# Performance work log

Hardware: AMD Instinct MI355X
Metric: run time of the kernel (lower is better)

## Reference

```python
import jax, jax.numpy as jnp
import numpy as np

K = 20
SLOPE = 0.2  # LeakyReLU negative slope used by DGCNN edge convs


def _knn_idx(x, k):
    # x: [C, N]. Returns [N, k] indices of nearest neighbors by L2 distance
    # (includes self), matching torch topk of -pairwise_dist.
    xx = jnp.sum(x * x, axis=0)                      # [N]
    neg_dist = 2.0 * (x.T @ x) - xx[:, None] - xx[None, :]  # [N, N]
    return jax.lax.top_k(neg_dist, k)[1]


def _graph_feature(x, k):
    # x: [C, N] -> edge features [2C, N, k] = concat(x_j - x_i, x_i)
    idx = _knn_idx(x, k)                             # [N, k]
    nb = x[:, idx]                                   # [C, N, k] gather
    xc = jnp.broadcast_to(x[:, :, None], nb.shape)   # [C, N, k]
    return jnp.concatenate([nb - xc, xc], axis=0)


def _edge_conv(x, w, s, c, k):
    # 1x1 Conv2d (no bias) + eval-mode BN folded into per-channel (s, c)
    # + LeakyReLU, then max over the k neighbors.
    f = _graph_feature(x, k)                         # [2C, N, k]
    y = jnp.einsum('oc,cnk->onk', w, f)              # [Co, N, k]
    y = jax.nn.leaky_relu(y * s[:, None, None] + c[:, None, None], SLOPE)
    return jnp.max(y, axis=-1)                       # [Co, N]


def setup_inputs() -> dict:
    key = jax.random.key(0)
    ks = jax.random.split(key, 25)
    N = 16384
    f32 = jnp.float32

    def w(k, shape):
        return jax.random.normal(k, shape, dtype=f32) * 0.05

    def scale(k, shape):
        return 1.0 + 0.1 * jax.random.uniform(k, shape, dtype=f32)

    return {
        'coords': jax.random.normal(ks[0], (N, 3), dtype=f32),
        'feats': jax.random.uniform(ks[1], (N, 1), dtype=f32),
        'w1': w(ks[2], (64, 8)),    's1': scale(ks[3], (64,)),  'c1': w(ks[4], (64,)),
        'w2': w(ks[5], (64, 128)),  's2': scale(ks[6], (64,)),  'c2': w(ks[7], (64,)),
        'w3': w(ks[8], (128, 128)), 's3': scale(ks[9], (128,)), 'c3': w(ks[10], (128,)),
        'w4': w(ks[11], (256, 256)),'s4': scale(ks[12], (256,)),'c4': w(ks[13], (256,)),
        'w5': w(ks[14], (512, 512)),'s5': scale(ks[15], (512,)),'c5': w(ks[16], (512,)),
        'wf': w(ks[17], (3, 256, 512)), 'sf': scale(ks[18], (3, 256)), 'cf': w(ks[19], (3, 256)),
        'wsem': w(ks[20], (20, 256)), 'bsem': w(ks[21], (20,)),
    }


def reference(coords, feats, w1, s1, c1, w2, s2, c2, w3, s3, c3,
              w4, s4, c4, w5, s5, c5, wf, sf, cf, wsem, bsem):
    # Single-cloud batch (batch_size=1): x_input = cat(coords, feats).T -> [4, N]
    x0 = jnp.concatenate([coords.T, feats.T], axis=0)        # [4, N]
    x1 = _edge_conv(x0, w1, s1, c1, K)                       # [64, N]
    x2 = _edge_conv(x1, w2, s2, c2, K)                       # [64, N]
    x3 = _edge_conv(x2, w3, s3, c3, K)                       # [128, N]
    x4 = _edge_conv(x3, w4, s4, c4, K)                       # [256, N]
    cat = jnp.concatenate([x1, x2, x3, x4], axis=0)          # [512, N]
    x5 = jax.nn.leaky_relu(
        jnp.einsum('oc,cn->on', w5, cat) * s5[:, None] + c5[:, None], SLOPE)

    # Multi-scale feat_layers + out_bn (eval-mode BN folded to sf, cf)
    ms_feats = (jnp.einsum('soc,cn->son', wf, x5)
                * sf[:, :, None] + cf[:, :, None])           # [3, 256, N]

    # sem_head on the last scale's features
    sem_feat = ms_feats[-1].T                                # [N, 256]
    sem_logits = (sem_feat @ wsem.T + bsem)[None]            # [1, N, 20]

    ms_coords = jnp.broadcast_to(coords[None], (3,) + coords.shape)  # [3, N, 3]
    ms_masks = jnp.zeros((3, coords.shape[0]), dtype=bool)           # [3, N]
    return ms_feats, ms_coords, ms_masks, sem_logits
```

## Files before the change

kernel.cpp:

```cpp
#include <hip/hip_runtime.h>
#include <hip/hip_bf16.h>
#include <cmath>

#define K_NN 20
#define SLOPE 0.2f
#define NSEG 8
#define TK 16
#define SCAP 8

__device__ __forceinline__ float lrelu(float x) { return x > 0.f ? x : SLOPE * x; }

__device__ __forceinline__ void topk_insert(float (&bd)[K_NN], int (&bi)[K_NN], float nd, int ji) {
  bool c[K_NN];
#pragma unroll
  for (int j = 0; j < K_NN; ++j) c[j] = nd > bd[j];
#pragma unroll
  for (int j = K_NN - 1; j >= 1; --j) {
    bd[j] = c[j] ? (c[j - 1] ? bd[j - 1] : nd) : bd[j];
    bi[j] = c[j] ? (c[j - 1] ? bi[j - 1] : ji) : bi[j];
  }
  bd[0] = c[0] ? nd : bd[0];
  bi[0] = c[0] ? ji : bi[0];
}

__global__ void build_x0_coords(const float* __restrict__ coords, const float* __restrict__ feats,
                                float* __restrict__ x0, float* __restrict__ oC,
                                float* __restrict__ oM, int N) {
  int n = blockIdx.x * 256 + threadIdx.x;
  if (n >= N) return;
  float c0 = coords[n * 3 + 0], c1 = coords[n * 3 + 1], c2 = coords[n * 3 + 2];
  float f = feats[n];
  float4 v = make_float4(c0, c1, c2, f);
  *(float4*)(x0 + (size_t)n * 4) = v;
#pragma unroll
  for (int s = 0; s < 3; ++s) {
    size_t b = (size_t)s * N * 3 + (size_t)n * 3;
    oC[b + 0] = c0; oC[b + 1] = c1; oC[b + 2] = c2;
    oM[(size_t)s * N + n] = 0.f;
  }
}

__global__ void compute_xx(const float* __restrict__ x, int ld, int C,
                           float* __restrict__ xx, int N) {
  int n = blockIdx.x * 256 + threadIdx.x;
  if (n >= N) return;
  const float* r = x + (size_t)n * ld;
  float s = 0.f;
  for (int c = 0; c < C; c += 4) {
    float4 v = *(const float4*)(r + c);
    s += v.x * v.x; s += v.y * v.y; s += v.z * v.z; s += v.w * v.w;
  }
  xx[n] = s;
}

template <int C>
__global__ __launch_bounds__(256, 2) void knn_seg(
    const float* __restrict__ xP, int ld, const float* __restrict__ xx,
    float* __restrict__ pd, int* __restrict__ pi, int N, int segLen) {
  constexpr int T = 64;
  __shared__ float tile[T * C];
  __shared__ float txx[T];
  __shared__ float sd_st[SCAP * 256];
  __shared__ int si_st[SCAP * 256];
  int tid = threadIdx.x;
  int q = blockIdx.x * 256 + tid;
  int j0 = blockIdx.y * segLen;

  float4 qv[C / 4];
#pragma unroll
  for (int c4 = 0; c4 < C / 4; ++c4) qv[c4] = *(const float4*)(xP + (size_t)q * ld + c4 * 4);
  float xxq = xx[q];

  float bd[K_NN]; int bi[K_NN];
#pragma unroll
  for (int k = 0; k < K_NN; ++k) { bd[k] = -INFINITY; bi[k] = 0; }
  float thr = -INFINITY;
  int cnt = 0;

  for (int jt = j0; jt < j0 + segLen; jt += T) {
    constexpr int TOT4 = T * C / 4;
    for (int f = tid; f < TOT4; f += 256) {
      int t = f / (C / 4), c4 = f % (C / 4);
      *(float4*)(tile + t * C + c4 * 4) = *(const float4*)(xP + (size_t)(jt + t) * ld + c4 * 4);
    }
    if (tid < T) txx[tid] = xx[jt + tid];
    __syncthreads();
#pragma unroll 2
    for (int t = 0; t < T; ++t) {
      const float4* rp = (const float4*)(tile + t * C);
      float dot = 0.f;
#pragma unroll
      for (int c4 = 0; c4 < C / 4; ++c4) {
        float4 v = rp[c4];
        dot += qv[c4].x * v.x; dot += qv[c4].y * v.y;
        dot += qv[c4].z * v.z; dot += qv[c4].w * v.w;
      }
      float nd = 2.f * dot - xxq - txx[t];
      if (nd > thr) {
        sd_st[cnt * 256 + tid] = nd;
        si_st[cnt * 256 + tid] = jt + t;
        cnt++;
      }
      if (__any(cnt == SCAP)) {
        for (int e = 0; e < cnt; ++e) {
          float dnd = sd_st[e * 256 + tid];
          int dji = si_st[e * 256 + tid];
          if (dnd > bd[K_NN - 1]) topk_insert(bd, bi, dnd, dji);
        }
        cnt = 0;
        thr = bd[K_NN - 1];
      }
    }
    __syncthreads();
  }
  for (int e = 0; e < cnt; ++e) {
    float dnd = sd_st[e * 256 + tid];
    int dji = si_st[e * 256 + tid];
    if (dnd > bd[K_NN - 1]) topk_insert(bd, bi, dnd, dji);
  }

  size_t base = ((size_t)blockIdx.y * N + q) * K_NN;
#pragma unroll
  for (int k = 0; k < K_NN; ++k) { pd[base + k] = bd[k]; pi[base + k] = bi[k]; }
}

__global__ void knn_merge(const float* __restrict__ pd, const int* __restrict__ pi,
                          int* __restrict__ idx, int N, int S) {
  int q = blockIdx.x * 256 + threadIdx.x;
  if (q >= N) return;
  float bd[K_NN]; int bi[K_NN];
#pragma unroll
  for (int k = 0; k < K_NN; ++k) { bd[k] = -INFINITY; bi[k] = 0; }
  for (int s = 0; s < S; ++s) {
    size_t base = ((size_t)s * N + q) * K_NN;
    for (int k = 0; k < K_NN; ++k) {
      float nd = pd[base + k];
      if (!(nd > bd[K_NN - 1])) break;
      topk_insert(bd, bi, nd, pi[base + k]);
    }
  }
#pragma unroll
  for (int k = 0; k < K_NN; ++k) idx[(size_t)q * K_NN + k] = bi[k];
}

__global__ void prep_wcat(const float* __restrict__ w, float* __restrict__ wcat, int O, int C) {
  int i = blockIdx.x * 256 + threadIdx.x;
  if (i >= O * C) return;
  int o = i / C, c = i % C;
  float wa = w[(size_t)o * 2 * C + c];
  float wb = w[(size_t)o * 2 * C + C + c];
  wcat[(size_t)o * C + c] = wa;
  wcat[((size_t)O + o) * C + c] = wb - wa;
}

template <int MODE>
__global__ __launch_bounds__(256) void gemm_nt(
    const float* __restrict__ A, int lda, const float* __restrict__ B, int ldb,
    float* __restrict__ Out, int ldo, int M, int Nout, int Kdim,
    const float* __restrict__ sv, const float* __restrict__ cv) {
  __shared__ float As[TK][64];
  __shared__ float Bs[TK][64];
  int tid = threadIdx.x;
  int tx = tid & 15, ty = tid >> 4;
  int m0 = blockIdx.x * 64, n0 = blockIdx.y * 64;
  int lrow = tid >> 2, lkq = tid & 3;
  float acc[4][4] = {};

  for (int k0 = 0; k0 < Kdim; k0 += TK) {
    float4 av = make_float4(0.f, 0.f, 0.f, 0.f), bv = make_float4(0.f, 0.f, 0.f, 0.f);
    if (k0 + lkq * 4 < Kdim) {
      av = *(const float4*)(A + (size_t)(m0 + lrow) * lda + k0 + lkq * 4);
      bv = *(const float4*)(B + (size_t)(n0 + lrow) * ldb + k0 + lkq * 4);
    }
    As[lkq * 4 + 0][lrow] = av.x; As[lkq * 4 + 1][lrow] = av.y;
    As[lkq * 4 + 2][lrow] = av.z; As[lkq * 4 + 3][lrow] = av.w;
    Bs[lkq * 4 + 0][lrow] = bv.x; Bs[lkq * 4 + 1][lrow] = bv.y;
    Bs[lkq * 4 + 2][lrow] = bv.z; Bs[lkq * 4 + 3][lrow] = bv.w;
    __syncthreads();
#pragma unroll
    for (int kk = 0; kk < TK; ++kk) {
      float a[4], b[4];
      *(float4*)a = *(const float4*)&As[kk][ty * 4];
      *(float4*)b = *(const float4*)&Bs[kk][tx * 4];
#pragma unroll
      for (int i = 0; i < 4; ++i)
#pragma unroll
        for (int j = 0; j < 4; ++j) acc[i][j] += a[i] * b[j];
    }
    __syncthreads();
  }

  float4 s4 = make_float4(1.f, 1.f, 1.f, 1.f), c4 = make_float4(0.f, 0.f, 0.f, 0.f);
  if (MODE != 0) {
    s4 = *(const float4*)(sv + n0 + tx * 4);
    c4 = *(const float4*)(cv + n0 + tx * 4);
  }
#pragma unroll
  for (int i = 0; i < 4; ++i) {
    float4 r = make_float4(acc[i][0], acc[i][1], acc[i][2], acc[i][3]);
    if (MODE != 0) {
      r.x = r.x * s4.x + c4.x; r.y = r.y * s4.y + c4.y;
      r.z = r.z * s4.z + c4.z; r.w = r.w * s4.w + c4.w;
    }
    if (MODE == 1) { r.x = lrelu(r.x); r.y = lrelu(r.y); r.z = lrelu(r.z); r.w = lrelu(r.w); }
    *(float4*)(Out + (size_t)(m0 + ty * 4 + i) * ldo + n0 + tx * 4) = r;
  }
}

template <int O>
__global__ void edge_max(const float* __restrict__ U, const int* __restrict__ idx,
                         const float* __restrict__ sv, const float* __restrict__ cv,
                         float* __restrict__ out, int N) {
  constexpr int TPP = O / 4;
  constexpr int PPB = 256 / TPP;
  int tid = threadIdx.x;
  int n = blockIdx.x * PPB + tid / TPP;
  int o4 = tid % TPP;
  const int* ir = idx + (size_t)n * K_NN;
  float4 m = make_float4(-INFINITY, -INFINITY, -INFINITY, -INFINITY);
#pragma unroll
  for (int k = 0; k < K_NN; ++k) {
    int j = ir[k];
    float4 t = *(const float4*)(U + (size_t)j * (2 * O) + o4 * 4);
    m.x = fmaxf(m.x, t.x); m.y = fmaxf(m.y, t.y);
    m.z = fmaxf(m.z, t.z); m.w = fmaxf(m.w, t.w);
  }
  float4 v = *(const float4*)(U + (size_t)n * (2 * O) + O + o4 * 4);
  float4 s4 = *(const float4*)(sv + o4 * 4);
  float4 c4 = *(const float4*)(cv + o4 * 4);
  float4 r;
  r.x = lrelu(s4.x * (v.x + m.x) + c4.x);
  r.y = lrelu(s4.y * (v.y + m.y) + c4.y);
  r.z = lrelu(s4.z * (v.z + m.z) + c4.z);
  r.w = lrelu(s4.w * (v.w + m.w) + c4.w);
  *(float4*)(out + (size_t)n * 512 + o4 * 4) = r;
}

__global__ void transpose_nt(const float* __restrict__ in, float* __restrict__ out, int N, int Cc) {
  __shared__ float t[32][33];
  int bx = blockIdx.x, by = blockIdx.y;
  int lx = threadIdx.x, ly = threadIdx.y;
#pragma unroll
  for (int i = 0; i < 4; ++i)
    t[ly + i * 8][lx] = in[(size_t)(by * 32 + ly + i * 8) * Cc + bx * 32 + lx];
  __syncthreads();
#pragma unroll
  for (int i = 0; i < 4; ++i)
    out[(size_t)(bx * 32 + ly + i * 8) * N + by * 32 + lx] = t[lx][ly + i * 8];
}

__global__ void sem_kernel(const float* __restrict__ T1, const float* __restrict__ wsem,
                           const float* __restrict__ bsem, float* __restrict__ out, int N) {
  int tid = threadIdx.x;
  int n = blockIdx.x * 8 + (tid >> 5);
  int g = tid & 31;
  if (g < 20) {
    const float* row = T1 + (size_t)n * 768 + 512;
    const float* wr = wsem + (size_t)g * 256;
    float acc = 0.f;
    for (int o = 0; o < 256; ++o) acc += row[o] * wr[o];
    out[(size_t)n * 20 + g] = acc + bsem[g];
  }
}

template <int C, int O>
static void run_layer(const float* x, int ld, const float* wc, const float* sv, const float* cv,
                      float* outcol, float* xxb, int* idxb, float* pd, int* pi, float* U,
                      int N, hipStream_t stream) {
  compute_xx<<<N / 256, 256, 0, stream>>>(x, ld, C, xxb, N);
  knn_seg<C><<<dim3(N / 256, NSEG), 256, 0, stream>>>(x, ld, xxb, pd, pi, N, N / NSEG);
  knn_merge<<<N / 256, 256, 0, stream>>>(pd, pi, idxb, N, NSEG);
  gemm_nt<0><<<dim3(N / 64, (2 * O) / 64), 256, 0, stream>>>(x, ld, wc, C, U, 2 * O, N, 2 * O, C,
                                                             nullptr, nullptr);
  edge_max<O><<<N / (256 / (O / 4)), 256, 0, stream>>>(U, idxb, sv, cv, outcol, N);
}

extern "C" void kernel_launch(void* const* d_in, const int* in_sizes, int n_in,
                              void* d_out, int out_size, void* d_ws, size_t ws_size,
                              hipStream_t stream) {
  const int N = in_sizes[0] / 3;
  const float* coords = (const float*)d_in[0];
  const float* feats  = (const float*)d_in[1];
  const float* w1 = (const float*)d_in[2];
  const float* s1 = (const float*)d_in[3];
  const float* c1 = (const float*)d_in[4];
  const float* w2 = (const float*)d_in[5];
  const float* s2 = (const float*)d_in[6];
  const float* c2 = (const float*)d_in[7];
  const float* w3 = (const float*)d_in[8];
  const float* s3 = (const float*)d_in[9];
  const float* c3 = (const float*)d_in[10];
  const float* w4 = (const float*)d_in[11];
  const float* s4 = (const float*)d_in[12];
  const float* c4 = (const float*)d_in[13];
  const float* w5 = (const float*)d_in[14];
  const float* s5 = (const float*)d_in[15];
  const float* c5 = (const float*)d_in[16];
  const float* wf = (const float*)d_in[17];
  const float* sf = (const float*)d_in[18];
  const float* cf = (const float*)d_in[19];
  const float* wsem = (const float*)d_in[20];
  const float* bsem = (const float*)d_in[21];

  float* base = (float*)d_ws;
  size_t off = 0;
  float* XC  = base + off; off += (size_t)N * 512;
  float* UX5 = base + off; off += (size_t)N * 512;
  float* x0  = base + off; off += (size_t)N * 4;
  float* xxb = base + off; off += (size_t)N;
  int*   idxb = (int*)(base + off); off += (size_t)N * K_NN;
  float* wc1 = base + off; off += 128 * 4;
  float* wc2 = base + off; off += 128 * 64;
  float* wc3 = base + off; off += 256 * 64;
  float* wc4 = base + off; off += 512 * 128;
  float* T1  = base + off; off += (size_t)N * 768;
  float* pd = T1;
  int*   pi = (int*)(T1 + (size_t)NSEG * N * K_NN);

  float* oF = (float*)d_out;
  float* oC = oF + (size_t)3 * 256 * N;
  float* oM = oC + (size_t)3 * N * 3;
  float* oL = oM + (size_t)3 * N;

  build_x0_coords<<<N / 256, 256, 0, stream>>>(coords, feats, x0, oC, oM, N);

  prep_wcat<<<(64 * 4 + 255) / 256, 256, 0, stream>>>(w1, wc1, 64, 4);
  prep_wcat<<<(64 * 64 + 255) / 256, 256, 0, stream>>>(w2, wc2, 64, 64);
  prep_wcat<<<(128 * 64 + 255) / 256, 256, 0, stream>>>(w3, wc3, 128, 64);
  prep_wcat<<<(256 * 128 + 255) / 256, 256, 0, stream>>>(w4, wc4, 256, 128);

  run_layer<4, 64>(x0, 4, wc1, s1, c1, XC + 0, xxb, idxb, pd, pi, UX5, N, stream);
  run_layer<64, 64>(XC + 0, 512, wc2, s2, c2, XC + 64, xxb, idxb, pd, pi, UX5, N, stream);
  run_layer<64, 128>(XC + 64, 512, wc3, s3, c3, XC + 128, xxb, idxb, pd, pi, UX5, N, stream);
  run_layer<128, 256>(XC + 128, 512, wc4, s4, c4, XC + 256, xxb, idxb, pd, pi, UX5, N, stream);

  gemm_nt<1><<<dim3(N / 64, 8), 256, 0, stream>>>(XC, 512, w5, 512, UX5, 512, N, 512, 512, s5, c5);
  gemm_nt<2><<<dim3(N / 64, 12), 256, 0, stream>>>(UX5, 512, wf, 512, T1, 768, N, 768, 512, sf, cf);
  transpose_nt<<<dim3(24, N / 32), dim3(32, 8), 0, stream>>>(T1, oF, N, 768);
  sem_kernel<<<N / 8, 256, 0, stream>>>(T1, wsem, bsem, oL, N);
}
```

Measured before the change: 4.684 ms.

## Add register-tiled shared-memory kNN kernel for high-dimensional edge-conv layers

Adds a knn_tile kernel that computes 64x64 query-candidate distance tiles with a 4x4 register-blocked dot product from swizzled shared memory. Only 64 threads of each block then scan the tile and maintain the running top-k through a staging buffer. Layers 2-4 (C=64/128) use it with 4 segments instead of 8, while layer 1 keeps the old per-query kernel. The aim is to cut global/LDS traffic per distance compared with the one-query-per-thread scan. The risk is that the selection step runs on only a quarter of the threads and becomes serialized.

```diff
diff --git a/kernel.cpp b/kernel.cpp
--- a/kernel.cpp
+++ b/kernel.cpp
@@ -5,6 +5,7 @@
 #define K_NN 20
 #define SLOPE 0.2f
 #define NSEG 8
+#define NSEG_T 4
 #define TK 16
 #define SCAP 8
 
@@ -124,6 +125,106 @@
   for (int k = 0; k < K_NN; ++k) { pd[base + k] = bd[k]; pi[base + k] = bi[k]; }
 }
 
+template <int C>
+__global__ __launch_bounds__(256) void knn_tile(
+    const float* __restrict__ xP, int ld, const float* __restrict__ xx,
+    float* __restrict__ pd, int* __restrict__ pi, int N, int segLen) {
+  constexpr int SQ4 = (C + 4) / 4;
+  __shared__ float4 Qs[64 * SQ4];
+  __shared__ float4 Cs[64 * SQ4];
+  __shared__ float dist[64 * 65];
+  __shared__ float qxx[64];
+  __shared__ float txx[64];
+  __shared__ float sd_st[SCAP * 64];
+  __shared__ int si_st[SCAP * 64];
+
+  int tid = threadIdx.x;
+  int tx = tid & 15, ty = tid >> 4;
+  int q0 = blockIdx.x * 64;
+  int j0 = blockIdx.y * segLen;
+
+  for (int p = tid; p < 64 * (C / 4); p += 256) {
+    int r = p / (C / 4), c4 = p % (C / 4);
+    Qs[r * SQ4 + (c4 ^ ((r >> 2) & 15))] =
+        *(const float4*)(xP + (size_t)(q0 + r) * ld + c4 * 4);
+  }
+  if (tid < 64) qxx[tid] = xx[q0 + tid];
+
+  float bd[K_NN]; int bi[K_NN];
+#pragma unroll
+  for (int k = 0; k < K_NN; ++k) { bd[k] = -INFINITY; bi[k] = 0; }
+  float thr = -INFINITY;
+  int cnt = 0;
+
+  for (int jt = j0; jt < j0 + segLen; jt += 64) {
+    for (int p = tid; p < 64 * (C / 4); p += 256) {
+      int r = p / (C / 4), c4 = p % (C / 4);
+      Cs[r * SQ4 + (c4 ^ ((r >> 2) & 15))] =
+          *(const float4*)(xP + (size_t)(jt + r) * ld + c4 * 4);
+    }
+    if (tid < 64) txx[tid] = xx[jt + tid];
+    __syncthreads();
+
+    float acc[4][4] = {};
+    for (int kc = 0; kc < C / 4; ++kc) {
+      float4 qa[4], ca[4];
+#pragma unroll
+      for (int i = 0; i < 4; ++i) qa[i] = Qs[(ty * 4 + i) * SQ4 + (kc ^ ty)];
+#pragma unroll
+      for (int j = 0; j < 4; ++j) ca[j] = Cs[(tx * 4 + j) * SQ4 + (kc ^ tx)];
+#pragma unroll
+      for (int i = 0; i < 4; ++i)
+#pragma unroll
+        for (int j = 0; j < 4; ++j) {
+          acc[i][j] += qa[i].x * ca[j].x;
+          acc[i][j] += qa[i].y * ca[j].y;
+          acc[i][j] += qa[i].z * ca[j].z;
+          acc[i][j] += qa[i].w * ca[j].w;
+        }
+    }
+#pragma unroll
+    for (int i = 0; i < 4; ++i) {
+      float xq = qxx[ty * 4 + i];
+#pragma unroll
+      for (int j = 0; j < 4; ++j)
+        dist[(ty * 4 + i) * 65 + tx * 4 + j] =
+            2.f * acc[i][j] - xq - txx[tx * 4 + j];
+    }
+    __syncthreads();
+
+    if (tid < 64) {
+      for (int j = 0; j < 64; ++j) {
+        float nd = dist[tid * 65 + j];
+        if (nd > thr) {
+          sd_st[cnt * 64 + tid] = nd;
+          si_st[cnt * 64 + tid] = jt + j;
+          cnt++;
+        }
+        if (__any(cnt == SCAP)) {
+          for (int e = 0; e < cnt; ++e) {
+            float dnd = sd_st[e * 64 + tid];
+            int dji = si_st[e * 64 + tid];
+            if (dnd > bd[K_NN - 1]) topk_insert(bd, bi, dnd, dji);
+          }
+          cnt = 0;
+          thr = bd[K_NN - 1];
+        }
+      }
+    }
+  }
+
+  if (tid < 64) {
+    for (int e = 0; e < cnt; ++e) {
+      float dnd = sd_st[e * 64 + tid];
+      int dji = si_st[e * 64 + tid];
+      if (dnd > bd[K_NN - 1]) topk_insert(bd, bi, dnd, dji);
+    }
+    size_t base = ((size_t)blockIdx.y * N + q0 + tid) * K_NN;
+#pragma unroll
+    for (int k = 0; k < K_NN; ++k) { pd[base + k] = bd[k]; pi[base + k] = bi[k]; }
+  }
+}
+
 __global__ void knn_merge(const float* __restrict__ pd, const int* __restrict__ pi,
                           int* __restrict__ idx, int N, int S) {
   int q = blockIdx.x * 256 + threadIdx.x;
@@ -264,12 +365,24 @@
 }
 
 template <int C, int O>
-static void run_layer(const float* x, int ld, const float* wc, const float* sv, const float* cv,
-                      float* outcol, float* xxb, int* idxb, float* pd, int* pi, float* U,
-                      int N, hipStream_t stream) {
+static void run_layer_seg(const float* x, int ld, const float* wc, const float* sv,
+                          const float* cv, float* outcol, float* xxb, int* idxb, float* pd,
+                          int* pi, float* U, int N, hipStream_t stream) {
   compute_xx<<<N / 256, 256, 0, stream>>>(x, ld, C, xxb, N);
   knn_seg<C><<<dim3(N / 256, NSEG), 256, 0, stream>>>(x, ld, xxb, pd, pi, N, N / NSEG);
   knn_merge<<<N / 256, 256, 0, stream>>>(pd, pi, idxb, N, NSEG);
+  gemm_nt<0><<<dim3(N / 64, (2 * O) / 64), 256, 0, stream>>>(x, ld, wc, C, U, 2 * O, N, 2 * O, C,
+                                                             nullptr, nullptr);
+  edge_max<O><<<N / (256 / (O / 4)), 256, 0, stream>>>(U, idxb, sv, cv, outcol, N);
+}
+
+template <int C, int O>
+static void run_layer_tile(const float* x, int ld, const float* wc, const float* sv,
+                           const float* cv, float* outcol, float* xxb, int* idxb, float* pd,
+                           int* pi, float* U, int N, hipStream_t stream) {
+  compute_xx<<<N / 256, 256, 0, stream>>>(x, ld, C, xxb, N);
+  knn_tile<C><<<dim3(N / 64, NSEG_T), 256, 0, stream>>>(x, ld, xxb, pd, pi, N, N / NSEG_T);
+  knn_merge<<<N / 256, 256, 0, stream>>>(pd, pi, idxb, N, NSEG_T);
   gemm_nt<0><<<dim3(N / 64, (2 * O) / 64), 256, 0, stream>>>(x, ld, wc, C, U, 2 * O, N, 2 * O, C,
                                                              nullptr, nullptr);
   edge_max<O><<<N / (256 / (O / 4)), 256, 0, stream>>>(U, idxb, sv, cv, outcol, N);
@@ -329,10 +442,10 @@
   prep_wcat<<<(128 * 64 + 255) / 256, 256, 0, stream>>>(w3, wc3, 128, 64);
   prep_wcat<<<(256 * 128 + 255) / 256, 256, 0, stream>>>(w4, wc4, 256, 128);
 
-  run_layer<4, 64>(x0, 4, wc1, s1, c1, XC + 0, xxb, idxb, pd, pi, UX5, N, stream);
-  run_layer<64, 64>(XC + 0, 512, wc2, s2, c2, XC + 64, xxb, idxb, pd, pi, UX5, N, stream);
-  run_layer<64, 128>(XC + 64, 512, wc3, s3, c3, XC + 128, xxb, idxb, pd, pi, UX5, N, stream);
-  run_layer<128, 256>(XC + 128, 512, wc4, s4, c4, XC + 256, xxb, idxb, pd, pi, UX5, N, stream);
+  run_layer_seg<4, 64>(x0, 4, wc1, s1, c1, XC + 0, xxb, idxb, pd, pi, UX5, N, stream);
+  run_layer_tile<64, 64>(XC + 0, 512, wc2, s2, c2, XC + 64, xxb, idxb, pd, pi, UX5, N, stream);
+  run_layer_tile<64, 128>(XC + 64, 512, wc3, s3, c3, XC + 128, xxb, idxb, pd, pi, UX5, N, stream);
+  run_layer_tile<128, 256>(XC + 128, 512, wc4, s4, c4, XC + 256, xxb, idxb, pd, pi, UX5, N, stream);
 
   gemm_nt<1><<<dim3(N / 64, 8), 256, 0, stream>>>(XC, 512, w5, 512, UX5, 512, N, 512, 512, s5, c5);
   gemm_nt<2><<<dim3(N / 64, 12), 256, 0, stream>>>(UX5, 512, wf, 512, T1, 768, N, 768, 512, sf, cf);
```

New measurement: 7.235 ms. +54.5%, slower.

## Compute kNN distances with split-fp16 MFMA and fused in-block top-k merge

Applied to the files above, without the earlier changes.

Layers 2-4 now compute kNN dot products on matrix cores, using a three-term fp16 hi/lo split to approximate fp32 accuracy. A new prep kernel builds the hi/lo halves, and the kNN kernel double-buffers swizzled candidate tiles through LDS. Each query's top-k is filtered by a running threshold and merged across the 8 partial lists inside the block, so the separate segment and merge kernels are no longer needed. This targets the scalar fp32 distance compute that dominates kNN time. The cost is extra prep passes and workspace aliasing, plus a small risk of neighbor ordering differing from the fp32 reference on near-ties.

```diff
diff --git a/kernel.cpp b/kernel.cpp
--- a/kernel.cpp
+++ b/kernel.cpp
@@ -7,6 +7,10 @@
 #define NSEG 8
 #define TK 16
 #define SCAP 8
+
+typedef _Float16 h8 __attribute__((ext_vector_type(8)));
+typedef _Float16 h4 __attribute__((ext_vector_type(4)));
+typedef float f4v __attribute__((ext_vector_type(4)));
 
 __device__ __forceinline__ float lrelu(float x) { return x > 0.f ? x : SLOPE * x; }
 
@@ -51,6 +55,23 @@
     s += v.x * v.x; s += v.y * v.y; s += v.z * v.z; s += v.w * v.w;
   }
   xx[n] = s;
+}
+
+template <int C>
+__global__ void prep_hl(const float* __restrict__ x, int ld, _Float16* __restrict__ xh,
+                        _Float16* __restrict__ xl, int N) {
+  constexpr int C4 = C / 4;
+  int i = blockIdx.x * 256 + threadIdx.x;
+  if (i >= N * C4) return;
+  int n = i / C4, c4 = i % C4;
+  float4 v = *(const float4*)(x + (size_t)n * ld + c4 * 4);
+  h4 hh, ll;
+  hh[0] = (_Float16)v.x; ll[0] = (_Float16)(v.x - (float)hh[0]);
+  hh[1] = (_Float16)v.y; ll[1] = (_Float16)(v.y - (float)hh[1]);
+  hh[2] = (_Float16)v.z; ll[2] = (_Float16)(v.z - (float)hh[2]);
+  hh[3] = (_Float16)v.w; ll[3] = (_Float16)(v.w - (float)hh[3]);
+  *(h4*)(xh + (size_t)n * C + c4 * 4) = hh;
+  *(h4*)(xl + (size_t)n * C + c4 * 4) = ll;
 }
 
 template <int C>
@@ -143,6 +164,179 @@
   for (int k = 0; k < K_NN; ++k) idx[(size_t)q * K_NN + k] = bi[k];
 }
 
+template <int C>
+__global__ __launch_bounds__(512, 2) void knn_mfma(
+    const _Float16* __restrict__ xh, const _Float16* __restrict__ xl,
+    const float* __restrict__ xx, int* __restrict__ idx, int N) {
+  constexpr int SLOTS = C / 8;
+  constexpr int SWM = SLOTS - 1;
+  constexpr int NCH = C / 32;
+  constexpr int TILE_UNITS = 2 * 32 * SLOTS;
+  constexpr int UPT = TILE_UNITS / 256;
+  constexpr int STAGE_B = 2 * 2 * TILE_UNITS * 16;
+  constexpr int MERGE_B = 64 * 8 * K_NN * 8;
+  constexpr int LDS_B = (STAGE_B + 32768 > MERGE_B) ? STAGE_B + 32768 : MERGE_B;
+  __shared__ char lds[LDS_B];
+  float* sd_st = (float*)(lds + STAGE_B);
+  int* si_st = (int*)(lds + STAGE_B + 16384);
+
+  int tid = threadIdx.x;
+  int wv = tid >> 6, lane = tid & 63;
+  int qh = wv >> 1, ch = wv & 1;
+  int lj = lane & 15, g = lane >> 4;
+  int q0 = blockIdx.x * 64;
+  int q = q0 + qh * 16 + lj;
+  int chbase = ch * (N / 2);
+  const int NT = (N / 2) / 32;
+
+  h8 bh[NCH], bl[NCH];
+#pragma unroll
+  for (int m = 0; m < NCH; ++m) {
+    bh[m] = *(const h8*)(xh + (size_t)q * C + m * 32 + g * 8);
+    bl[m] = *(const h8*)(xl + (size_t)q * C + m * 32 + g * 8);
+  }
+  float qxx = xx[q];
+
+  float bd[K_NN]; int bi[K_NN];
+#pragma unroll
+  for (int k = 0; k < K_NN; ++k) { bd[k] = -INFINITY; bi[k] = 0; }
+  float thr = -INFINITY;
+  int cnt = 0;
+
+  int cidx = qh * 64 + lane;
+  float4 ldr[UPT];
+
+  auto ldreg = [&](int t) {
+    int jt = chbase + t * 32;
+#pragma unroll
+    for (int u = 0; u < UPT; ++u) {
+      int p = cidx * UPT + u;
+      int part = p / (32 * SLOTS);
+      int row = (p / SLOTS) & 31;
+      int slot = p & SWM;
+      const _Float16* src = part ? xl : xh;
+      ldr[u] = *(const float4*)(src + (size_t)(jt + row) * C + (slot ^ (row & SWM)) * 8);
+    }
+  };
+  auto dswrite = [&](int buf) {
+#pragma unroll
+    for (int u = 0; u < UPT; ++u) {
+      int p = cidx * UPT + u;
+      *(float4*)(lds + ((size_t)(ch * 2 + buf) * TILE_UNITS + p) * 16) = ldr[u];
+    }
+  };
+  auto compute = [&](int buf, int jt) {
+    float cxx[8];
+#pragma unroll
+    for (int s = 0; s < 2; ++s)
+#pragma unroll
+      for (int r = 0; r < 4; ++r) cxx[s * 4 + r] = xx[jt + s * 16 + g * 4 + r];
+    char* tb = lds + (size_t)(ch * 2 + buf) * TILE_UNITS * 16;
+#pragma unroll
+    for (int sub = 0; sub < 2; ++sub) {
+      int row = sub * 16 + lj;
+      h8 ah[NCH], al[NCH];
+#pragma unroll
+      for (int m = 0; m < NCH; ++m) {
+        int su = (m * 4 + g) ^ (row & SWM);
+        ah[m] = *(const h8*)(tb + ((size_t)(0 * 32 + row) * SLOTS + su) * 16);
+        al[m] = *(const h8*)(tb + ((size_t)(1 * 32 + row) * SLOTS + su) * 16);
+      }
+      f4v acc = {0.f, 0.f, 0.f, 0.f};
+#pragma unroll
+      for (int m = 0; m < NCH; ++m)
+        acc = __builtin_amdgcn_mfma_f32_16x16x32_f16(ah[m], bh[m], acc, 0, 0, 0);
+#pragma unroll
+      for (int m = 0; m < NCH; ++m)
+        acc = __builtin_amdgcn_mfma_f32_16x16x32_f16(ah[m], bl[m], acc, 0, 0, 0);
+#pragma unroll
+      for (int m = 0; m < NCH; ++m)
+        acc = __builtin_amdgcn_mfma_f32_16x16x32_f16(al[m], bh[m], acc, 0, 0, 0);
+#pragma unroll
+      for (int r = 0; r < 4; ++r) {
+        float d = 2.f * acc[r] - qxx - cxx[sub * 4 + r];
+        if (d > thr) {
+          sd_st[cnt * 512 + tid] = d;
+          si_st[cnt * 512 + tid] = jt + sub * 16 + g * 4 + r;
+          cnt++;
+        }
+        if (__any(cnt == SCAP)) {
+          for (int e = 0; e < cnt; ++e) {
+            float dnd = sd_st[e * 512 + tid];
+            int dji = si_st[e * 512 + tid];
+            if (dnd > bd[K_NN - 1]) topk_insert(bd, bi, dnd, dji);
+          }
+          cnt = 0;
+          thr = bd[K_NN - 1];
+        }
+      }
+    }
+  };
+
+  ldreg(0);
+  dswrite(0);
+  __syncthreads();
+  for (int t = 0; t < NT; ++t) {
+    int cur = t & 1;
+    if (t + 1 < NT) ldreg(t + 1);
+    compute(cur, chbase + t * 32);
+    __syncthreads();
+    if (t + 1 < NT) {
+      dswrite(cur ^ 1);
+      __syncthreads();
+    }
+  }
+  for (int e = 0; e < cnt; ++e) {
+    float dnd = sd_st[e * 512 + tid];
+    int dji = si_st[e * 512 + tid];
+    if (dnd > bd[K_NN - 1]) topk_insert(bd, bi, dnd, dji);
+  }
+  __syncthreads();
+
+  float* mg = (float*)lds;
+  int list = ch * 4 + g;
+  int qlocal = qh * 16 + lj;
+#pragma unroll
+  for (int k = 0; k < K_NN; ++k) {
+    int e = ((qlocal * 8 + list) * K_NN + k) * 2;
+    mg[e] = bd[k];
+    ((int*)mg)[e + 1] = bi[k];
+  }
+  __syncthreads();
+  if (tid < 64) {
+    int pr[8] = {0, 0, 0, 0, 0, 0, 0, 0};
+    float hd[8]; int hx[8];
+#pragma unroll
+    for (int j = 0; j < 8; ++j) {
+      int e = ((tid * 8 + j) * K_NN) * 2;
+      hd[j] = mg[e]; hx[j] = ((int*)mg)[e + 1];
+    }
+    for (int k = 0; k < K_NN; ++k) {
+      float best = hd[0]; int bidx = hx[0]; int bj = 0;
+#pragma unroll
+      for (int j = 1; j < 8; ++j) {
+        bool btr = (hd[j] > best) || (hd[j] == best && hx[j] < bidx);
+        best = btr ? hd[j] : best;
+        bidx = btr ? hx[j] : bidx;
+        bj = btr ? j : bj;
+      }
+      idx[(size_t)(q0 + tid) * K_NN + k] = bidx;
+#pragma unroll
+      for (int j = 0; j < 8; ++j) {
+        if (j == bj) {
+          pr[j]++;
+          if (pr[j] < K_NN) {
+            int e = ((tid * 8 + j) * K_NN + pr[j]) * 2;
+            hd[j] = mg[e]; hx[j] = ((int*)mg)[e + 1];
+          } else {
+            hd[j] = -INFINITY; hx[j] = 0x7fffffff;
+          }
+        }
+      }
+    }
+  }
+}
+
 __global__ void prep_wcat(const float* __restrict__ w, float* __restrict__ wcat, int O, int C) {
   int i = blockIdx.x * 256 + threadIdx.x;
   if (i >= O * C) return;
@@ -264,12 +458,24 @@
 }
 
 template <int C, int O>
-static void run_layer(const float* x, int ld, const float* wc, const float* sv, const float* cv,
-                      float* outcol, float* xxb, int* idxb, float* pd, int* pi, float* U,
-                      int N, hipStream_t stream) {
+static void run_layer_seg(const float* x, int ld, const float* wc, const float* sv,
+                          const float* cv, float* outcol, float* xxb, int* idxb, float* pd,
+                          int* pi, float* U, int N, hipStream_t stream) {
   compute_xx<<<N / 256, 256, 0, stream>>>(x, ld, C, xxb, N);
   knn_seg<C><<<dim3(N / 256, NSEG), 256, 0, stream>>>(x, ld, xxb, pd, pi, N, N / NSEG);
   knn_merge<<<N / 256, 256, 0, stream>>>(pd, pi, idxb, N, NSEG);
+  gemm_nt<0><<<dim3(N / 64, (2 * O) / 64), 256, 0, stream>>>(x, ld, wc, C, U, 2 * O, N, 2 * O, C,
+                                                             nullptr, nullptr);
+  edge_max<O><<<N / (256 / (O / 4)), 256, 0, stream>>>(U, idxb, sv, cv, outcol, N);
+}
+
+template <int C, int O>
+static void run_layer_mfma(const float* x, int ld, const float* wc, const float* sv,
+                           const float* cv, float* outcol, float* xxb, int* idxb,
+                           _Float16* xh, _Float16* xl, float* U, int N, hipStream_t stream) {
+  compute_xx<<<N / 256, 256, 0, stream>>>(x, ld, C, xxb, N);
+  prep_hl<C><<<(N * (C / 4)) / 256, 256, 0, stream>>>(x, ld, xh, xl, N);
+  knn_mfma<C><<<N / 64, 512, 0, stream>>>(xh, xl, xxb, idxb, N);
   gemm_nt<0><<<dim3(N / 64, (2 * O) / 64), 256, 0, stream>>>(x, ld, wc, C, U, 2 * O, N, 2 * O, C,
                                                              nullptr, nullptr);
   edge_max<O><<<N / (256 / (O / 4)), 256, 0, stream>>>(U, idxb, sv, cv, outcol, N);
@@ -316,6 +522,8 @@
   float* T1  = base + off; off += (size_t)N * 768;
   float* pd = T1;
   int*   pi = (int*)(T1 + (size_t)NSEG * N * K_NN);
+  _Float16* xh = (_Float16*)UX5;
+  _Float16* xl = (_Float16*)(UX5 + (size_t)N * 64);
 
   float* oF = (float*)d_out;
   float* oC = oF + (size_t)3 * 256 * N;
@@ -329,10 +537,10 @@
   prep_wcat<<<(128 * 64 + 255) / 256, 256, 0, stream>>>(w3, wc3, 128, 64);
   prep_wcat<<<(256 * 128 + 255) / 256, 256, 0, stream>>>(w4, wc4, 256, 128);
 
-  run_layer<4, 64>(x0, 4, wc1, s1, c1, XC + 0, xxb, idxb, pd, pi, UX5, N, stream);
-  run_layer<64, 64>(XC + 0, 512, wc2, s2, c2, XC + 64, xxb, idxb, pd, pi, UX5, N, stream);
-  run_layer<64, 128>(XC + 64, 512, wc3, s3, c3, XC + 128, xxb, idxb, pd, pi, UX5, N, stream);
-  run_layer<128, 256>(XC + 128, 512, wc4, s4, c4, XC + 256, xxb, idxb, pd, pi, UX5, N, stream);
+  run_layer_seg<4, 64>(x0, 4, wc1, s1, c1, XC + 0, xxb, idxb, pd, pi, UX5, N, stream);
+  run_layer_mfma<64, 64>(XC + 0, 512, wc2, s2, c2, XC + 64, xxb, idxb, xh, xl, UX5, N, stream);
+  run_layer_mfma<64, 128>(XC + 64, 512, wc3, s3, c3, XC + 128, xxb, idxb, xh, xl, UX5, N, stream);
+  run_layer_mfma<128, 256>(XC + 128, 512, wc4, s4, c4, XC + 256, xxb, idxb, xh, xl, UX5, N, stream);
 
   gemm_nt<1><<<dim3(N / 64, 8), 256, 0, stream>>>(XC, 512, w5, 512, UX5, 512, N, 512, 512, s5, c5);
   gemm_nt<2><<<dim3(N / 64, 12), 256, 0, stream>>>(UX5, 512, wf, 512, T1, 768, N, 768, 512, sf, cf);
```

After: 4.065 ms. 13.2% less time.
